# Kernel tuning notes

Hardware: AMD Instinct MI355X
Metric: run time of the kernel (lower is better)

## Reference

```python
import jax, jax.numpy as jnp
import numpy as np

S, D_IN, N_RULES, N_OUT = 8192, 1024, 16, 512  # batch, in_features, num_rules, out_features


def setup_inputs() -> dict:
    key = jax.random.key(0)
    k1, k2, k3, k4 = jax.random.split(key, 4)
    X = jax.random.normal(k1, (S, D_IN), dtype=jnp.float32)
    # fc layer weight/bias after add_neurons: out_features = N_RULES * N_OUT
    W = jax.random.normal(k2, (N_RULES * N_OUT, D_IN), dtype=jnp.float32) / np.sqrt(D_IN).astype(np.float32)
    b = jax.random.normal(k3, (N_RULES * N_OUT,), dtype=jnp.float32) * 0.01
    # rule firing strengths from Layer (computed under no_grad in the original)
    lambdas = jax.random.uniform(k4, (S, N_RULES), dtype=jnp.float32)
    return {"X": X, "W": W, "b": b, "lambdas": lambdas}


def reference(X, W, b, lambdas):
    # X: [S, D_IN]; W: [R*O, D_IN]; b: [R*O]; lambdas: [S, R]
    H = jax.nn.sigmoid(X @ W.T + b)                       # [S, R*O]
    Hr = H.reshape(H.shape[0], lambdas.shape[1], N_OUT)   # [S, R, O] (block n = cols n*O:(n+1)*O)
    # apply_rule_strength: out[s,o] = sum_r lambdas[s,r] * H[s, r*O + o]
    return jnp.einsum('sr,sro->so', lambdas, Hr)          # [S, O]
```

## Files before the change

### kernel.cpp

```cpp
#include <hip/hip_runtime.h>
#include <hip/hip_bf16.h>
#include <stdint.h>

#define SS 8192
#define DD 1024
#define RR 16
#define OO 512

typedef __bf16 bf16_8 __attribute__((ext_vector_type(8)));
typedef float f32_4 __attribute__((ext_vector_type(4)));
typedef int i32_4 __attribute__((ext_vector_type(4)));

typedef __attribute__((address_space(1))) void g1_void;
typedef __attribute__((address_space(3))) void lds_void;

#define L2E 1.44269504f

__device__ __forceinline__ void gload_lds16(const void* g, void* l) {
  __builtin_amdgcn_global_load_lds((g1_void*)(uintptr_t)g,
                                   (lds_void*)(uint32_t)(uintptr_t)l, 16, 0, 0);
}

__global__ __launch_bounds__(256) void somfnn_quant(
    const float* __restrict__ X, const float* __restrict__ W,
    char* __restrict__ Xq, char* __restrict__ Wq,
    float* __restrict__ sX, float* __restrict__ sW, float4* __restrict__ out) {
  const int tid = threadIdx.x;
  const int wv = tid >> 6;
  const int l = tid & 63;
  const int r = blockIdx.x * 4 + wv;
  const bool isX = r < SS;
  const float* src = isX ? (X + (size_t)r * DD) : (W + (size_t)(r - SS) * DD);
  char* dst = isX ? (Xq + (size_t)r * DD) : (Wq + (size_t)(r - SS) * DD);

  const float4* s4 = (const float4*)src;
  float4 v[4];
#pragma unroll
  for (int c = 0; c < 4; ++c) v[c] = s4[c * 64 + l];

  out[(size_t)blockIdx.x * 256 + tid] = float4{0.f, 0.f, 0.f, 0.f};

  float m = 0.f;
#pragma unroll
  for (int c = 0; c < 4; ++c)
    m = fmaxf(m, fmaxf(fmaxf(fabsf(v[c].x), fabsf(v[c].y)),
                       fmaxf(fabsf(v[c].z), fabsf(v[c].w))));
#pragma unroll
  for (int off = 32; off > 0; off >>= 1) m = fmaxf(m, __shfl_xor(m, off, 64));
  m = fmaxf(m, 1e-20f);

  const float inv = 127.0f / m;
  int* di = (int*)dst;
#pragma unroll
  for (int c = 0; c < 4; ++c) {
    int q0 = __float2int_rn(v[c].x * inv);
    int q1 = __float2int_rn(v[c].y * inv);
    int q2 = __float2int_rn(v[c].z * inv);
    int q3 = __float2int_rn(v[c].w * inv);
    di[c * 64 + l] = (q0 & 0xff) | ((q1 & 0xff) << 8) | ((q2 & 0xff) << 16) |
                     ((q3 & 0xff) << 24);
  }
  if (l == 0) {
    if (isX) sX[r] = m / 127.0f;
    else sW[r - SS] = m / 127.0f;
  }
}

__global__ __launch_bounds__(256, 2) void somfnn_gemm_i8(
    const char* __restrict__ Xq, const char* __restrict__ Wq,
    const float* __restrict__ sX, const float* __restrict__ sW,
    const float* __restrict__ bias_g, const float* __restrict__ lam_g,
    float* __restrict__ out) {
  constexpr int BM = 128, BN = 128, BK = 64;
  constexpr int TILEB = BM * BK;
  constexpr int NSTEP = 8 * (DD / BK);

  __shared__ __align__(16) char lds_a[3][TILEB];
  __shared__ __align__(16) char lds_b[3][TILEB];
  __shared__ float lds_bias[8 * BN];
  __shared__ float lds_lam[8 * BM];
  __shared__ float lds_sB[8 * BN];
  __shared__ float lds_sA[BM];

  const int tid = threadIdx.x;
  const int bid = blockIdx.x;

  const int l = tid & 63;
  const int w = tid >> 6;
  const int lane15 = l & 15;
  const int q = l >> 4;
  const int wm = w >> 1;
  const int wn = w & 1;

  const int xcd = bid & 7;
  const int chunk = bid >> 3;
  const int sb = xcd * 8 + (chunk & 7);
  const int ob = (chunk >> 3) & 3;
  const int rhalf = chunk >> 5;
  const int s0 = sb * BM;
  const int o0 = ob * BN;
  const int r0 = rhalf * 8;

  for (int idx = tid; idx < 8 * BN; idx += 256) {
    int rr = idx >> 7, j = idx & 127;
    lds_bias[idx] = -L2E * bias_g[(r0 + rr) * OO + o0 + j];
    lds_sB[idx] = sW[(r0 + rr) * OO + o0 + j];
  }
  for (int idx = tid; idx < 8 * BM; idx += 256) {
    int rr = idx >> 7, i = idx & 127;
    lds_lam[idx] = lam_g[(s0 + i) * RR + (r0 + rr)];
  }
  if (tid < BM) lds_sA[tid] = sX[s0 + tid];

  int goffs[2];
#pragma unroll
  for (int i = 0; i < 2; ++i) {
    int cc = (w * 2 + i) * 64 + l;
    int row = cc >> 2;
    int lc = cc & 3;
    goffs[i] = row * DD + ((lc ^ ((row >> 1) & 3)) * 16);
  }

  int afo[4], bfo[4];
#pragma unroll
  for (int t = 0; t < 4; ++t) {
    int ra = wm * 64 + t * 16 + lane15;
    afo[t] = ra * BK + ((q ^ ((ra >> 1) & 3)) * 16);
    int rb = wn * 64 + t * 16 + lane15;
    bfo[t] = rb * BK + ((q ^ ((rb >> 1) & 3)) * 16);
  }

  auto issue_pre = [&](int step, int buf) {
    int rl = step >> 4, kt = step & 15;
    const char* ga = Xq + (size_t)s0 * DD + kt * BK;
    const char* gb = Wq + ((size_t)(r0 + rl) * OO + o0) * DD + kt * BK;
#pragma unroll
    for (int i = 0; i < 2; ++i)
      gload_lds16(ga + goffs[i], &lds_a[buf][(w * 2 + i) * 1024]);
#pragma unroll
    for (int i = 0; i < 2; ++i)
      gload_lds16(gb + goffs[i], &lds_b[buf][(w * 2 + i) * 1024]);
  };

  i32_4 acc[4][4];
  f32_4 oacc[4][4];
#pragma unroll
  for (int mi = 0; mi < 4; ++mi)
#pragma unroll
    for (int ni = 0; ni < 4; ++ni) {
      acc[mi][ni] = i32_4{0, 0, 0, 0};
      oacc[mi][ni] = f32_4{0.f, 0.f, 0.f, 0.f};
    }

  asm volatile("s_waitcnt vmcnt(0)" ::: "memory");
  issue_pre(0, 0);
  issue_pre(1, 1);
  asm volatile("s_waitcnt vmcnt(4) lgkmcnt(0)" ::: "memory");
  __builtin_amdgcn_sched_barrier(0);
  __builtin_amdgcn_s_barrier();
  __builtin_amdgcn_sched_barrier(0);

  for (int step = 0; step < NSTEP; ++step) {
    const int cur = step % 3;
    const bool more = (step + 2) < NSTEP;
    if (more) issue_pre(step + 2, (step + 2) % 3);

    const char* A = lds_a[cur];
    const char* B = lds_b[cur];
    i32_4 av[4], bv[4];
#pragma unroll
    for (int mi = 0; mi < 4; ++mi) av[mi] = *(const i32_4*)(A + afo[mi]);
#pragma unroll
    for (int ni = 0; ni < 4; ++ni) bv[ni] = *(const i32_4*)(B + bfo[ni]);
#pragma unroll
    for (int mi = 0; mi < 4; ++mi)
#pragma unroll
      for (int ni = 0; ni < 4; ++ni)
        acc[mi][ni] =
            __builtin_amdgcn_mfma_i32_16x16x64_i8(av[mi], bv[ni], acc[mi][ni], 0, 0, 0);

    if ((step & 15) == 15) {
      const int rl = step >> 4;
      float lsa[4][4], lamv[4][4];
#pragma unroll
      for (int mi = 0; mi < 4; ++mi)
#pragma unroll
        for (int v = 0; v < 4; ++v) {
          int ridx = wm * 64 + mi * 16 + q * 4 + v;
          lsa[mi][v] = -L2E * lds_sA[ridx];
          lamv[mi][v] = lds_lam[rl * BM + ridx];
        }
#pragma unroll
      for (int ni = 0; ni < 4; ++ni) {
        const int cidx = wn * 64 + ni * 16 + lane15;
        const float nb = lds_bias[rl * BN + cidx];
        const float sbv = lds_sB[rl * BN + cidx];
#pragma unroll
        for (int mi = 0; mi < 4; ++mi)
#pragma unroll
          for (int v = 0; v < 4; ++v) {
            float t = __builtin_fmaf((float)acc[mi][ni][v], lsa[mi][v] * sbv, nb);
            float e = __builtin_amdgcn_exp2f(t);
            float h = __builtin_amdgcn_rcpf(1.0f + e);
            oacc[mi][ni][v] = __builtin_fmaf(lamv[mi][v], h, oacc[mi][ni][v]);
            acc[mi][ni][v] = 0;
          }
      }
    }

    if (more) {
      asm volatile("s_waitcnt vmcnt(4) lgkmcnt(0)" ::: "memory");
    } else {
      asm volatile("s_waitcnt vmcnt(0) lgkmcnt(0)" ::: "memory");
    }
    __builtin_amdgcn_sched_barrier(0);
    __builtin_amdgcn_s_barrier();
    __builtin_amdgcn_sched_barrier(0);
  }

#pragma unroll
  for (int mi = 0; mi < 4; ++mi)
#pragma unroll
    for (int ni = 0; ni < 4; ++ni)
#pragma unroll
      for (int v = 0; v < 4; ++v) {
        int row = s0 + wm * 64 + mi * 16 + q * 4 + v;
        int col = o0 + wn * 64 + ni * 16 + lane15;
        atomicAdd(&out[row * OO + col], oacc[mi][ni][v]);
      }
}

__global__ __launch_bounds__(256, 2) void somfnn_gemm_fb(
    const float* __restrict__ Xf32, const float* __restrict__ Wf32,
    const float* __restrict__ bias_g, const float* __restrict__ lam_g,
    float* __restrict__ out) {
  constexpr int BM = 128, BN = 128, BK = 64;
  constexpr int TILE = BM * BK;
  constexpr int NSTEP = 8 * (DD / BK);

  __shared__ __align__(16) __bf16 lds_a[2][TILE];
  __shared__ __align__(16) __bf16 lds_b[2][TILE];
  __shared__ float lds_bias[8 * BN];
  __shared__ float lds_lam[8 * BM];

  const int tid = threadIdx.x;
  const int bid = blockIdx.x;
  const int l = tid & 63;
  const int w = tid >> 6;
  const int lane15 = l & 15;
  const int q = l >> 4;
  const int wm = w >> 1;
  const int wn = w & 1;

  const int xcd = bid & 7;
  const int chunk = bid >> 3;
  const int sb = xcd * 8 + (chunk & 7);
  const int ob = (chunk >> 3) & 3;
  const int rhalf = chunk >> 5;
  const int s0 = sb * BM;
  const int o0 = ob * BN;
  const int r0 = rhalf * 8;

  for (int idx = tid; idx < 8 * BN; idx += 256) {
    int rr = idx >> 7, j = idx & 127;
    lds_bias[idx] = -L2E * bias_g[(r0 + rr) * OO + o0 + j];
  }
  for (int idx = tid; idx < 8 * BM; idx += 256) {
    int rr = idx >> 7, i = idx & 127;
    lds_lam[idx] = lam_g[(s0 + i) * RR + (r0 + rr)];
  }

  int goffs[4], coffs[4];
#pragma unroll
  for (int i = 0; i < 4; ++i) {
    int c = (w * 4 + i) * 64 + l;
    int row = c >> 3;
    int k8 = (c & 7) ^ (row & 7);
    goffs[i] = row * DD + k8 * 8;
    coffs[i] = c * 8;
  }
  int afo[4], bfo[4];
#pragma unroll
  for (int t = 0; t < 4; ++t) {
    int ra = wm * 64 + t * 16 + lane15;
    afo[t] = (ra * 8 + (q ^ (ra & 7))) * 8;
    int rb = wn * 64 + t * 16 + lane15;
    bfo[t] = (rb * 8 + (q ^ (rb & 7))) * 8;
  }

  float4 ra_[4][2], rb_[4][2];
  auto issue_fb = [&](int step) {
    int rl = step >> 4, kt = step & 15;
    const float* ga = Xf32 + s0 * DD + kt * BK;
    const float* gb = Wf32 + ((r0 + rl) * OO + o0) * DD + kt * BK;
#pragma unroll
    for (int i = 0; i < 4; ++i) {
      const float4* p = (const float4*)(ga + goffs[i]);
      ra_[i][0] = p[0]; ra_[i][1] = p[1];
      const float4* pb = (const float4*)(gb + goffs[i]);
      rb_[i][0] = pb[0]; rb_[i][1] = pb[1];
    }
  };
  auto commit_fb = [&](int buf) {
#pragma unroll
    for (int i = 0; i < 4; ++i) {
      bf16_8 t;
      t[0] = (__bf16)ra_[i][0].x; t[1] = (__bf16)ra_[i][0].y;
      t[2] = (__bf16)ra_[i][0].z; t[3] = (__bf16)ra_[i][0].w;
      t[4] = (__bf16)ra_[i][1].x; t[5] = (__bf16)ra_[i][1].y;
      t[6] = (__bf16)ra_[i][1].z; t[7] = (__bf16)ra_[i][1].w;
      *(bf16_8*)&lds_a[buf][coffs[i]] = t;
      bf16_8 u;
      u[0] = (__bf16)rb_[i][0].x; u[1] = (__bf16)rb_[i][0].y;
      u[2] = (__bf16)rb_[i][0].z; u[3] = (__bf16)rb_[i][0].w;
      u[4] = (__bf16)rb_[i][1].x; u[5] = (__bf16)rb_[i][1].y;
      u[6] = (__bf16)rb_[i][1].z; u[7] = (__bf16)rb_[i][1].w;
      *(bf16_8*)&lds_b[buf][coffs[i]] = u;
    }
  };

  f32_4 acc[4][4], oacc[4][4];
#pragma unroll
  for (int mi = 0; mi < 4; ++mi)
#pragma unroll
    for (int ni = 0; ni < 4; ++ni) {
      acc[mi][ni] = f32_4{0.f, 0.f, 0.f, 0.f};
      oacc[mi][ni] = f32_4{0.f, 0.f, 0.f, 0.f};
    }

  issue_fb(0);
  commit_fb(0);
  __syncthreads();

  for (int step = 0; step < NSTEP; ++step) {
    const int cur = step & 1;
    const bool more = (step + 1) < NSTEP;
    if (more) issue_fb(step + 1);

    const __bf16* A = lds_a[cur];
    const __bf16* B = lds_b[cur];
#pragma unroll
    for (int ks = 0; ks < 2; ++ks) {
      const int xr = ks ? 32 : 0;
      bf16_8 av[4], bv[4];
#pragma unroll
      for (int mi = 0; mi < 4; ++mi) av[mi] = *(const bf16_8*)(A + (afo[mi] ^ xr));
#pragma unroll
      for (int ni = 0; ni < 4; ++ni) bv[ni] = *(const bf16_8*)(B + (bfo[ni] ^ xr));
#pragma unroll
      for (int mi = 0; mi < 4; ++mi)
#pragma unroll
        for (int ni = 0; ni < 4; ++ni)
          acc[mi][ni] =
              __builtin_amdgcn_mfma_f32_16x16x32_bf16(av[mi], bv[ni], acc[mi][ni], 0, 0, 0);
    }
    if (more) commit_fb(cur ^ 1);

    if ((step & 15) == 15) {
      const int rl = step >> 4;
      float lamv[4][4];
#pragma unroll
      for (int mi = 0; mi < 4; ++mi)
#pragma unroll
        for (int v = 0; v < 4; ++v)
          lamv[mi][v] = lds_lam[rl * BM + wm * 64 + mi * 16 + q * 4 + v];
#pragma unroll
      for (int ni = 0; ni < 4; ++ni) {
        const float nb = lds_bias[rl * BN + wn * 64 + ni * 16 + lane15];
#pragma unroll
        for (int mi = 0; mi < 4; ++mi)
#pragma unroll
          for (int v = 0; v < 4; ++v) {
            float t = __builtin_fmaf(acc[mi][ni][v], -L2E, nb);
            float e = __builtin_amdgcn_exp2f(t);
            float h = __builtin_amdgcn_rcpf(1.0f + e);
            oacc[mi][ni][v] = __builtin_fmaf(lamv[mi][v], h, oacc[mi][ni][v]);
            acc[mi][ni][v] = 0.f;
          }
      }
    }
    __syncthreads();
  }

#pragma unroll
  for (int mi = 0; mi < 4; ++mi)
#pragma unroll
    for (int ni = 0; ni < 4; ++ni)
#pragma unroll
      for (int v = 0; v < 4; ++v) {
        int row = s0 + wm * 64 + mi * 16 + q * 4 + v;
        int col = o0 + wn * 64 + ni * 16 + lane15;
        atomicAdd(&out[row * OO + col], oacc[mi][ni][v]);
      }
}

extern "C" void kernel_launch(void* const* d_in, const int* in_sizes, int n_in,
                              void* d_out, int out_size, void* d_ws, size_t ws_size,
                              hipStream_t stream) {
  const float* X = (const float*)d_in[0];
  const float* W = (const float*)d_in[1];
  const float* b = (const float*)d_in[2];
  const float* lam = (const float*)d_in[3];
  float* out = (float*)d_out;

  const size_t qbytes = (size_t)SS * DD;
  const size_t need = 2 * qbytes + 2 * (size_t)SS * sizeof(float);
  if (ws_size >= need) {
    char* Xq = (char*)d_ws;
    char* Wq = Xq + qbytes;
    float* sX = (float*)(Wq + qbytes);
    float* sW = sX + SS;
    somfnn_quant<<<dim3(4096), dim3(256), 0, stream>>>(X, W, Xq, Wq, sX, sW, (float4*)out);
    somfnn_gemm_i8<<<dim3(512), dim3(256), 0, stream>>>(Xq, Wq, sX, sW, b, lam, out);
  } else {
    hipMemsetAsync(out, 0, (size_t)SS * OO * sizeof(float), stream);
    somfnn_gemm_fb<<<dim3(512), dim3(256), 0, stream>>>(X, W, b, lam, out);
  }
}
```

Measured before the change: 204.4 us.

## Enlarge int8 GEMM tile to 256 rows with 8 waves and split-phase pipeline

The int8 GEMM block tile grows from 128x128 to 256x128, with 512 threads (8 waves) and half as many blocks, so each W tile loaded into LDS is reused across more rows. The main loop is split into two phases, each interleaving an A or B prefetch with a half of the MFMA work. The MFMA sections are wrapped in s_setprio, with an extra barrier between the phases. This aims to cut global/LDS traffic per FLOP and overlap loads with compute, at the cost of more LDS per block, higher register pressure and an extra sync per step.

New measurement: 207.6 us. About the same (+1.6%).

```diff
diff --git a/kernel.cpp b/kernel.cpp
--- a/kernel.cpp
+++ b/kernel.cpp
@@ -66,20 +66,19 @@
   }
 }
 
-__global__ __launch_bounds__(256, 2) void somfnn_gemm_i8(
+__global__ __launch_bounds__(512, 2) void somfnn_gemm_i8(
     const char* __restrict__ Xq, const char* __restrict__ Wq,
     const float* __restrict__ sX, const float* __restrict__ sW,
     const float* __restrict__ bias_g, const float* __restrict__ lam_g,
     float* __restrict__ out) {
-  constexpr int BM = 128, BN = 128, BK = 64;
-  constexpr int TILEB = BM * BK;
+  constexpr int BM = 256, BN = 128, BK = 64;
   constexpr int NSTEP = 8 * (DD / BK);
 
-  __shared__ __align__(16) char lds_a[3][TILEB];
-  __shared__ __align__(16) char lds_b[3][TILEB];
+  __shared__ __align__(16) char lds_a[3][BM * BK];
+  __shared__ __align__(16) char lds_b[3][BN * BK];
   __shared__ float lds_bias[8 * BN];
+  __shared__ float lds_sB[8 * BN];
   __shared__ float lds_lam[8 * BM];
-  __shared__ float lds_sB[8 * BN];
   __shared__ float lds_sA[BM];
 
   const int tid = threadIdx.x;
@@ -94,31 +93,38 @@
 
   const int xcd = bid & 7;
   const int chunk = bid >> 3;
-  const int sb = xcd * 8 + (chunk & 7);
-  const int ob = (chunk >> 3) & 3;
-  const int rhalf = chunk >> 5;
+  const int sb = xcd * 4 + (chunk & 3);
+  const int ob = (chunk >> 2) & 3;
+  const int rhalf = chunk >> 4;
   const int s0 = sb * BM;
   const int o0 = ob * BN;
   const int r0 = rhalf * 8;
 
-  for (int idx = tid; idx < 8 * BN; idx += 256) {
+  for (int idx = tid; idx < 8 * BN; idx += 512) {
     int rr = idx >> 7, j = idx & 127;
     lds_bias[idx] = -L2E * bias_g[(r0 + rr) * OO + o0 + j];
     lds_sB[idx] = sW[(r0 + rr) * OO + o0 + j];
   }
-  for (int idx = tid; idx < 8 * BM; idx += 256) {
-    int rr = idx >> 7, i = idx & 127;
+  for (int idx = tid; idx < 8 * BM; idx += 512) {
+    int rr = idx >> 8, i = idx & 255;
     lds_lam[idx] = lam_g[(s0 + i) * RR + (r0 + rr)];
   }
   if (tid < BM) lds_sA[tid] = sX[s0 + tid];
 
-  int goffs[2];
-#pragma unroll
-  for (int i = 0; i < 2; ++i) {
-    int cc = (w * 2 + i) * 64 + l;
+  int aoff[2];
+#pragma unroll
+  for (int g = 0; g < 2; ++g) {
+    int cc = w * 128 + g * 64 + l;
     int row = cc >> 2;
-    int lc = cc & 3;
-    goffs[i] = row * DD + ((lc ^ ((row >> 1) & 3)) * 16);
+    int kc = (cc & 3) ^ ((row >> 1) & 3);
+    aoff[g] = row * DD + kc * 16;
+  }
+  int boff;
+  {
+    int cc = w * 64 + l;
+    int row = cc >> 2;
+    int kc = (cc & 3) ^ ((row >> 1) & 3);
+    boff = row * DD + kc * 16;
   }
 
   int afo[4], bfo[4];
@@ -130,16 +136,20 @@
     bfo[t] = rb * BK + ((q ^ ((rb >> 1) & 3)) * 16);
   }
 
-  auto issue_pre = [&](int step, int buf) {
+  const char* gA = Xq + (size_t)s0 * DD;
+  const char* gB = Wq + ((size_t)r0 * OO + o0) * DD;
+
+  auto issueA = [&](int step, int buf) {
     int rl = step >> 4, kt = step & 15;
-    const char* ga = Xq + (size_t)s0 * DD + kt * BK;
-    const char* gb = Wq + ((size_t)(r0 + rl) * OO + o0) * DD + kt * BK;
-#pragma unroll
-    for (int i = 0; i < 2; ++i)
-      gload_lds16(ga + goffs[i], &lds_a[buf][(w * 2 + i) * 1024]);
-#pragma unroll
-    for (int i = 0; i < 2; ++i)
-      gload_lds16(gb + goffs[i], &lds_b[buf][(w * 2 + i) * 1024]);
+    (void)rl;
+    const char* ga = gA + kt * BK;
+    gload_lds16(ga + aoff[0], &lds_a[buf][w * 2048]);
+    gload_lds16(ga + aoff[1], &lds_a[buf][w * 2048 + 1024]);
+  };
+  auto issueB = [&](int step, int buf) {
+    int rl = step >> 4, kt = step & 15;
+    const char* gb = gB + (size_t)rl * OO * DD + kt * BK;
+    gload_lds16(gb + boff, &lds_b[buf][w * 1024]);
   };
 
   i32_4 acc[4][4];
@@ -152,32 +162,54 @@
       oacc[mi][ni] = f32_4{0.f, 0.f, 0.f, 0.f};
     }
 
-  asm volatile("s_waitcnt vmcnt(0)" ::: "memory");
-  issue_pre(0, 0);
-  issue_pre(1, 1);
-  asm volatile("s_waitcnt vmcnt(4) lgkmcnt(0)" ::: "memory");
+  issueA(0, 0); issueB(0, 0);
+  issueA(1, 1); issueB(1, 1);
+  asm volatile("s_waitcnt vmcnt(3) lgkmcnt(0)" ::: "memory");
   __builtin_amdgcn_sched_barrier(0);
   __builtin_amdgcn_s_barrier();
   __builtin_amdgcn_sched_barrier(0);
 
   for (int step = 0; step < NSTEP; ++step) {
     const int cur = step % 3;
-    const bool more = (step + 2) < NSTEP;
-    if (more) issue_pre(step + 2, (step + 2) % 3);
+    const int nxt = (step + 2) % 3;
+    const bool pre = (step + 2) < NSTEP;
 
     const char* A = lds_a[cur];
     const char* B = lds_b[cur];
     i32_4 av[4], bv[4];
-#pragma unroll
-    for (int mi = 0; mi < 4; ++mi) av[mi] = *(const i32_4*)(A + afo[mi]);
+
+    av[0] = *(const i32_4*)(A + afo[0]);
+    av[1] = *(const i32_4*)(A + afo[1]);
 #pragma unroll
     for (int ni = 0; ni < 4; ++ni) bv[ni] = *(const i32_4*)(B + bfo[ni]);
-#pragma unroll
-    for (int mi = 0; mi < 4; ++mi)
-#pragma unroll
-      for (int ni = 0; ni < 4; ++ni)
-        acc[mi][ni] =
-            __builtin_amdgcn_mfma_i32_16x16x64_i8(av[mi], bv[ni], acc[mi][ni], 0, 0, 0);
+    if (pre) issueA(step + 2, nxt);
+    asm volatile("s_waitcnt lgkmcnt(0)" ::: "memory");
+    __builtin_amdgcn_sched_barrier(0);
+    __builtin_amdgcn_s_setprio(1);
+#pragma unroll
+    for (int ni = 0; ni < 4; ++ni)
+      acc[0][ni] = __builtin_amdgcn_mfma_i32_16x16x64_i8(av[0], bv[ni], acc[0][ni], 0, 0, 0);
+#pragma unroll
+    for (int ni = 0; ni < 4; ++ni)
+      acc[1][ni] = __builtin_amdgcn_mfma_i32_16x16x64_i8(av[1], bv[ni], acc[1][ni], 0, 0, 0);
+    __builtin_amdgcn_s_setprio(0);
+    __builtin_amdgcn_sched_barrier(0);
+    __builtin_amdgcn_s_barrier();
+    __builtin_amdgcn_sched_barrier(0);
+
+    av[2] = *(const i32_4*)(A + afo[2]);
+    av[3] = *(const i32_4*)(A + afo[3]);
+    if (pre) issueB(step + 2, nxt);
+    asm volatile("s_waitcnt lgkmcnt(0)" ::: "memory");
+    __builtin_amdgcn_sched_barrier(0);
+    __builtin_amdgcn_s_setprio(1);
+#pragma unroll
+    for (int ni = 0; ni < 4; ++ni)
+      acc[2][ni] = __builtin_amdgcn_mfma_i32_16x16x64_i8(av[2], bv[ni], acc[2][ni], 0, 0, 0);
+#pragma unroll
+    for (int ni = 0; ni < 4; ++ni)
+      acc[3][ni] = __builtin_amdgcn_mfma_i32_16x16x64_i8(av[3], bv[ni], acc[3][ni], 0, 0, 0);
+    __builtin_amdgcn_s_setprio(0);
 
     if ((step & 15) == 15) {
       const int rl = step >> 4;
@@ -208,10 +240,10 @@
       }
     }
 
-    if (more) {
-      asm volatile("s_waitcnt vmcnt(4) lgkmcnt(0)" ::: "memory");
-    } else {
-      asm volatile("s_waitcnt vmcnt(0) lgkmcnt(0)" ::: "memory");
+    if (pre) {
+      asm volatile("s_waitcnt vmcnt(3)" ::: "memory");
+    } else if (step + 1 < NSTEP) {
+      asm volatile("s_waitcnt vmcnt(0)" ::: "memory");
     }
     __builtin_amdgcn_sched_barrier(0);
     __builtin_amdgcn_s_barrier();
@@ -411,7 +443,7 @@
     float* sX = (float*)(Wq + qbytes);
     float* sW = sX + SS;
     somfnn_quant<<<dim3(4096), dim3(256), 0, stream>>>(X, W, Xq, Wq, sX, sW, (float4*)out);
-    somfnn_gemm_i8<<<dim3(512), dim3(256), 0, stream>>>(Xq, Wq, sX, sW, b, lam, out);
+    somfnn_gemm_i8<<<dim3(256), dim3(512), 0, stream>>>(Xq, Wq, sX, sW, b, lam, out);
   } else {
     hipMemsetAsync(out, 0, (size_t)SS * OO * sizeof(float), stream);
     somfnn_gemm_fb<<<dim3(512), dim3(256), 0, stream>>>(X, W, b, lam, out);
```
